# Kernel optimization log

Hardware: AMD Instinct MI355X
Metric: run time of the kernel (lower is better)

Reference implementation:

```python
import jax, jax.numpy as jnp
import numpy as np

G = 128          # resolution
NE = 4           # n_emotions
SIGMA = 0.05     # splat kernel width
ETA = 0.01       # global write strength
ALPHA_H = 0.002
ALPHA_E = 0.001
LEAK = 5e-05
RADIUS = max(2, int(3.0 * SIGMA * G / 2.0))   # = 9
W = 2 * RADIUS + 1                            # = 19


def _laplacian(x):
    # 6-neighbor Laplacian with replicate padding; x: [..., G, G, G]
    pad = [(0, 0)] * (x.ndim - 3) + [(1, 1)] * 3
    p = jnp.pad(x, pad, mode='edge')
    c = p[..., 1:-1, 1:-1, 1:-1]
    return (p[..., :-2, 1:-1, 1:-1] + p[..., 2:, 1:-1, 1:-1]
            + p[..., 1:-1, :-2, 1:-1] + p[..., 1:-1, 2:, 1:-1]
            + p[..., 1:-1, 1:-1, :-2] + p[..., 1:-1, 1:-1, 2:]
            - 6.0 * c)


def _splat(H, E, positions, intensities, emotions):
    # Gaussian splat scatter-add into H [G,G,G] and E [NE,G,G,G].
    gp = (positions + 1.0) * 0.5 * (G - 1)                       # [N,3] grid coords
    c = jnp.clip(jnp.floor(gp).astype(jnp.int32), 0, G - 1)      # center cell
    offs = jnp.arange(-RADIUS, RADIUS + 1, dtype=jnp.int32)
    coords = c[:, :, None] + offs[None, None, :]                 # [N,3,W]
    valid = (coords >= 0) & (coords < G)
    cc = jnp.clip(coords, 0, G - 1)
    sig = SIGMA * G / 2.0
    d = coords.astype(gp.dtype) - gp[:, :, None]                 # [N,3,W]
    k1 = jnp.where(valid, jnp.exp(-(d * d) / (2.0 * sig * sig)), 0.0)
    kx, ky, kz = k1[:, 0], k1[:, 1], k1[:, 2]                    # [N,W] each (separable)
    omega = intensities * ETA                                    # [N]
    vals = (omega[:, None, None, None] * kx[:, :, None, None]
            * ky[:, None, :, None] * kz[:, None, None, :])       # [N,W,W,W]
    flat = ((cc[:, 0][:, :, None, None] * G + cc[:, 1][:, None, :, None]) * G
            + cc[:, 2][:, None, None, :]).reshape(-1)            # [N*W^3]
    H_new = H.reshape(-1).at[flat].add(vals.reshape(-1)).reshape(G, G, G)
    E_ch = []
    for e in range(NE):
        ve = (vals * emotions[:, e][:, None, None, None]).reshape(-1)
        E_ch.append(E[e].reshape(-1).at[flat].add(ve).reshape(G, G, G))
    return H_new, jnp.stack(E_ch)


def _step(H, E):
    H2 = jnp.maximum(H * (1.0 - LEAK) + ALPHA_H * _laplacian(H), 0.0)
    E2 = jnp.maximum(E * (1.0 - LEAK) + LEAK + ALPHA_E * _laplacian(E), 0.0)
    return H2, E2


def _sample(H, E, sp):
    # grid_sample trilinear, padding_mode='border', align_corners=True.
    # grid_sample axis convention: sp[...,0]->last axis, sp[...,1]->middle, sp[...,2]->first.
    B, T, _ = sp.shape
    t = jnp.clip((sp.reshape(-1, 3) + 1.0) * 0.5 * (G - 1), 0.0, G - 1)  # [BT,3]
    i0 = jnp.floor(t).astype(jnp.int32)
    f = t - i0
    i0 = jnp.clip(i0, 0, G - 1)
    i1 = jnp.clip(i0 + 1, 0, G - 1)
    x0, y0, z0 = i0[:, 0], i0[:, 1], i0[:, 2]
    x1, y1, z1 = i1[:, 0], i1[:, 1], i1[:, 2]
    fx, fy, fz = f[:, 0], f[:, 1], f[:, 2]

    def interp(vol):  # vol [..., G,G,G] -> [..., BT]
        out = 0.0
        for zi, wz in ((z0, 1.0 - fz), (z1, fz)):
            for yi, wy in ((y0, 1.0 - fy), (y1, fy)):
                for xi, wx in ((x0, 1.0 - fx), (x1, fx)):
                    out = out + vol[..., zi, yi, xi] * (wz * wy * wx)
        return out

    p_H = interp(H).reshape(B, T)
    p_E = interp(E).T.reshape(B, T, NE)
    return p_H, p_E


def setup_inputs() -> dict:
    key = jax.random.key(0)
    k1, k2, k3, k4 = jax.random.split(key, 4)
    N, B, T = 4096, 8, 1024
    return {
        'positions': jax.random.uniform(k1, (N, 3), jnp.float32, -0.95, 0.95),
        'intensities': jax.random.uniform(k2, (N,), jnp.float32),
        'emotions': jax.random.uniform(k3, (N, NE), jnp.float32),
        'sample_positions': jax.random.uniform(k4, (B, T, 3), jnp.float32, -1.0, 1.0),
        'H0': jnp.zeros((G, G, G), jnp.float32),
        'E0': jnp.ones((NE, G, G, G), jnp.float32),
    }


def reference(positions, intensities, emotions, sample_positions, H0, E0):
    H, E = _splat(H0, E0, positions, intensities, emotions)
    H, E = _step(H, E)
    p_H, p_E = _sample(H, E, sample_positions)
    return jnp.concatenate([p_H[..., None], p_E], axis=-1)  # [B,T,1+NE]
```

## Files before the change

### kernel.cpp

```cpp
#include <hip/hip_runtime.h>


namespace {
constexpr int   G      = 128;
constexpr int   G3     = G * G * G;
constexpr int   RAD    = 9;
constexpr float SIG    = 0.05f * (float)G * 0.5f;
constexpr float INV2S2 = 1.0f / (2.0f * SIG * SIG);
constexpr float ETA    = 0.01f;
constexpr float A_H    = 0.002f;
constexpr float A_E    = 0.001f;
constexpr float LEAK   = 5e-5f;

constexpr int T0 = 8, T1 = 4, T2 = 16;
constexpr int NT0 = G / T0, NT1 = G / T1, NT2 = G / T2;
constexpr int NTILES = NT0 * NT1 * NT2;
constexpr int CAP  = 96;
constexpr int CSTR = 32;
}

__device__ __forceinline__ int clampi(int v, int lo, int hi) {
    return min(max(v, lo), hi);
}

__global__ void __launch_bounds__(256) bin_meta_kernel(
        const float* __restrict__ pos, const float* __restrict__ inten,
        const float4* __restrict__ emo4,
        int* __restrict__ counts, int* __restrict__ lists,
        float4* __restrict__ meta, int N) {
    const int p    = blockIdx.x * 4 + (threadIdx.x >> 6);
    const int lane = threadIdx.x & 63;
    if (p >= N) return;

    const float gx = (pos[p * 3 + 0] + 1.0f) * 0.5f * (float)(G - 1);
    const float gy = (pos[p * 3 + 1] + 1.0f) * 0.5f * (float)(G - 1);
    const float gz = (pos[p * 3 + 2] + 1.0f) * 0.5f * (float)(G - 1);
    const int c0 = clampi((int)floorf(gx), 0, G - 1);
    const int c1 = clampi((int)floorf(gy), 0, G - 1);
    const int c2 = clampi((int)floorf(gz), 0, G - 1);

    if (lane == 0) {
        meta[2 * p]     = make_float4(gx, gy, gz, inten[p] * ETA);
        meta[2 * p + 1] = emo4[p];
    }

    const int t0lo = (max(c0 - 18, 0) + T0 - 1) >> 3;
    const int t0hi = min(c0 + 10, G - 1) >> 3;
    const int t1lo = (max(c1 - 14, 0) + T1 - 1) >> 2;
    const int t1hi = min(c1 + 10, G - 1) >> 2;
    const int t2lo = (max(c2 - 26, 0) + T2 - 1) >> 4;
    const int t2hi = min(c2 + 10, G - 1) >> 4;
    const int n0 = t0hi - t0lo, n1 = t1hi - t1lo, n2 = t2hi - t2lo;

    for (int s = lane; s < 84; s += 64) {
        const int a  = s / 21;
        const int r  = s - a * 21;
        const int b  = r / 3;
        const int cs = r - b * 3;
        if (a <= n0 && b <= n1 && cs <= n2) {
            const int t = ((t0lo + a) * NT1 + (t1lo + b)) * NT2 + (t2lo + cs);
            const int slot = atomicAdd(&counts[t * CSTR], 1);
            if (slot < CAP) lists[t * CAP + slot] = p;
        }
    }
}

__device__ __forceinline__ float stepped_at(const float* __restrict__ vol,
                                            int z, int y, int x,
                                            float addc, float alpha) {
    const int zm = max(z - 1, 0), zp = min(z + 1, G - 1);
    const int ym = max(y - 1, 0), yp = min(y + 1, G - 1);
    const int xm = max(x - 1, 0), xp = min(x + 1, G - 1);
    const float cv  = vol[(z * G + y) * G + x];
    const float lap = vol[(zm * G + y) * G + x] + vol[(zp * G + y) * G + x]
                    + vol[(z * G + ym) * G + x] + vol[(z * G + yp) * G + x]
                    + vol[(z * G + y) * G + xm] + vol[(z * G + y) * G + xp]
                    - 6.0f * cv;
    return cv * (1.0f - LEAK) + addc + alpha * lap;
}

__device__ __forceinline__ void axis_eval(float g, int ia, int ib,
        int ma, int pa, int mb, int pb, float wa, float wb,
        float& dir, float& lap) {
    const int cp = clampi((int)floorf(g), 0, G - 1);
    auto kf = [&](int v) -> float {
        const float d = (float)v - g;
        const float e = __expf(-d * d * INV2S2);
        return (abs(v - cp) <= RAD) ? e : 0.0f;
    };
    const float ka = kf(ia), kb = kf(ib);
    lap = wa * (kf(ma) + kf(pa) - 2.0f * ka)
        + wb * (kf(mb) + kf(pb) - 2.0f * kb);
    dir = wa * ka + wb * kb;
}

__global__ void __launch_bounds__(256) fused_sample_kernel(
        const float* __restrict__ sp, const float4* __restrict__ meta,
        const int* __restrict__ counts, const int* __restrict__ lists,
        const float* __restrict__ H0, const float* __restrict__ E0,
        float* __restrict__ out, int n_samp) {
    const int wave = (blockIdx.x * blockDim.x + threadIdx.x) >> 6;
    const int lane = threadIdx.x & 63;
    if (wave >= n_samp) return;

    const float s0 = sp[wave * 3 + 0];
    const float s1 = sp[wave * 3 + 1];
    const float s2 = sp[wave * 3 + 2];
    const float uz = fminf(fmaxf((s2 + 1.0f) * 0.5f * (float)(G - 1), 0.0f), (float)(G - 1));
    const float uy = fminf(fmaxf((s1 + 1.0f) * 0.5f * (float)(G - 1), 0.0f), (float)(G - 1));
    const float ux = fminf(fmaxf((s0 + 1.0f) * 0.5f * (float)(G - 1), 0.0f), (float)(G - 1));
    const int za = (int)floorf(uz); const float fz = uz - (float)za;
    const int ya = (int)floorf(uy); const float fy = uy - (float)ya;
    const int xa = (int)floorf(ux); const float fx = ux - (float)xa;
    const int zb = min(za + 1, G - 1);
    const int yb = min(ya + 1, G - 1);
    const int xb = min(xa + 1, G - 1);

    float bv = 0.0f;
    if (lane < 40) {
        const int c = lane >> 3, corner = lane & 7;
        const int d0 = corner & 1, d1 = (corner >> 1) & 1, d2 = corner >> 2;
        const int x = d0 ? xb : xa, y = d1 ? yb : ya, z = d2 ? zb : za;
        const float w = (d0 ? fx : 1.0f - fx) * (d1 ? fy : 1.0f - fy)
                      * (d2 ? fz : 1.0f - fz);
        const float* vol  = (c == 0) ? H0 : E0 + (size_t)(c - 1) * G3;
        const float addc  = (c == 0) ? 0.0f : LEAK;
        const float alpha = (c == 0) ? A_H : A_E;
        bv = w * stepped_at(vol, z, y, x, addc, alpha);
    }
    bv += __shfl_xor(bv, 1);
    bv += __shfl_xor(bv, 2);
    bv += __shfl_xor(bv, 4);

    const int tile = ((za >> 3) * NT1 + (ya >> 2)) * NT2 + (xa >> 4);
    const int cnt = min(counts[tile * CSTR], CAP);
    const int* __restrict__ lst = lists + tile * CAP;

    const int zma = max(za - 1, 0), zpa = min(za + 1, G - 1);
    const int zmb = max(zb - 1, 0), zpb = min(zb + 1, G - 1);
    const int yma = max(ya - 1, 0), ypa = min(ya + 1, G - 1);
    const int ymb = max(yb - 1, 0), ypb = min(yb + 1, G - 1);
    const int xma = max(xa - 1, 0), xpa = min(xa + 1, G - 1);
    const int xmb = max(xb - 1, 0), xpb = min(xb + 1, G - 1);
    const float wza = 1.0f - fz, wzb = fz;
    const float wya = 1.0f - fy, wyb = fy;
    const float wxa = 1.0f - fx, wxb = fx;

    float aH = 0.0f, aE0 = 0.0f, aE1 = 0.0f, aE2 = 0.0f, aE3 = 0.0f;
    for (int nb = lane; nb < cnt; nb += 64) {
        const int p = lst[nb];
        const float4 mg = meta[2 * p];
        const float4 me = meta[2 * p + 1];
        float dz_, lz_, dy_, ly_, dx_, lx_;
        axis_eval(mg.x, za, zb, zma, zpa, zmb, zpb, wza, wzb, dz_, lz_);
        axis_eval(mg.y, ya, yb, yma, ypa, ymb, ypb, wya, wyb, dy_, ly_);
        axis_eval(mg.z, xa, xb, xma, xpa, xmb, xpb, wxa, wxb, dx_, lx_);
        const float b3 = dz_ * dy_ * dx_;
        const float l3 = lz_ * dy_ * dx_ + dz_ * ly_ * dx_ + dz_ * dy_ * lx_;
        const float cH = mg.w * ((1.0f - LEAK) * b3 + A_H * l3);
        const float cE = mg.w * ((1.0f - LEAK) * b3 + A_E * l3);
        aH  += cH;
        aE0 += cE * me.x;  aE1 += cE * me.y;
        aE2 += cE * me.z;  aE3 += cE * me.w;
    }

#define RED64(v) { v += __shfl_xor(v, 1);  v += __shfl_xor(v, 2);  \
                   v += __shfl_xor(v, 4);  v += __shfl_xor(v, 8);  \
                   v += __shfl_xor(v, 16); v += __shfl_xor(v, 32); }
    RED64(aH) RED64(aE0) RED64(aE1) RED64(aE2) RED64(aE3)
#undef RED64

    const int  src   = (lane < 5) ? lane * 8 : 0;
    const float basec = __shfl(bv, src);
    const float sv = (lane == 0) ? aH  : (lane == 1) ? aE0
                   : (lane == 2) ? aE1 : (lane == 3) ? aE2 : aE3;
    if (lane < 5) out[wave * 5 + lane] = basec + sv;
}

extern "C" void kernel_launch(void* const* d_in, const int* in_sizes, int n_in,
                              void* d_out, int out_size, void* d_ws, size_t ws_size,
                              hipStream_t stream) {
    const float* positions   = (const float*)d_in[0];
    const float* intensities = (const float*)d_in[1];
    const float* emotions    = (const float*)d_in[2];
    const float* sample_pos  = (const float*)d_in[3];
    const float* H0          = (const float*)d_in[4];
    const float* E0          = (const float*)d_in[5];
    float* out = (float*)d_out;

    const int N = in_sizes[0] / 3;

    int*    counts = (int*)d_ws;
    int*    lists  = counts + (size_t)NTILES * CSTR;
    float4* meta   = (float4*)(lists + (size_t)NTILES * CAP);

    hipMemsetAsync(counts, 0, (size_t)NTILES * CSTR * sizeof(int), stream);

    bin_meta_kernel<<<(N + 3) / 4, 256, 0, stream>>>(
        positions, intensities, (const float4*)emotions, counts, lists, meta, N);

    const int n_samp = out_size / 5;
    fused_sample_kernel<<<(n_samp + 3) / 4, 256, 0, stream>>>(
        sample_pos, meta, counts, lists, H0, E0, out, n_samp);
}
```

Measured before the change: 113.8 us.

## Move base-field sampling into binning kernel and trim splat-axis exp evaluations

Merges the binning work and the sampling of the stepped base volumes (H0/E0 Laplacian with interpolation) into one launch, using separate block ranges. This lets the memory-bound base gathers overlap with the atomic binning, and the second kernel then only adds splat contributions into the output with a read-modify-write. The per-axis kernel evaluation now reuses shared neighbour values, cutting six exponentials per axis down to four. The cost is an extra global read-modify-write of the output and the base-sample coordinate math done twice.

```diff
diff --git a/kernel.cpp b/kernel.cpp
--- a/kernel.cpp
+++ b/kernel.cpp
@@ -21,48 +21,6 @@
 
 __device__ __forceinline__ int clampi(int v, int lo, int hi) {
     return min(max(v, lo), hi);
-}
-
-__global__ void __launch_bounds__(256) bin_meta_kernel(
-        const float* __restrict__ pos, const float* __restrict__ inten,
-        const float4* __restrict__ emo4,
-        int* __restrict__ counts, int* __restrict__ lists,
-        float4* __restrict__ meta, int N) {
-    const int p    = blockIdx.x * 4 + (threadIdx.x >> 6);
-    const int lane = threadIdx.x & 63;
-    if (p >= N) return;
-
-    const float gx = (pos[p * 3 + 0] + 1.0f) * 0.5f * (float)(G - 1);
-    const float gy = (pos[p * 3 + 1] + 1.0f) * 0.5f * (float)(G - 1);
-    const float gz = (pos[p * 3 + 2] + 1.0f) * 0.5f * (float)(G - 1);
-    const int c0 = clampi((int)floorf(gx), 0, G - 1);
-    const int c1 = clampi((int)floorf(gy), 0, G - 1);
-    const int c2 = clampi((int)floorf(gz), 0, G - 1);
-
-    if (lane == 0) {
-        meta[2 * p]     = make_float4(gx, gy, gz, inten[p] * ETA);
-        meta[2 * p + 1] = emo4[p];
-    }
-
-    const int t0lo = (max(c0 - 18, 0) + T0 - 1) >> 3;
-    const int t0hi = min(c0 + 10, G - 1) >> 3;
-    const int t1lo = (max(c1 - 14, 0) + T1 - 1) >> 2;
-    const int t1hi = min(c1 + 10, G - 1) >> 2;
-    const int t2lo = (max(c2 - 26, 0) + T2 - 1) >> 4;
-    const int t2hi = min(c2 + 10, G - 1) >> 4;
-    const int n0 = t0hi - t0lo, n1 = t1hi - t1lo, n2 = t2hi - t2lo;
-
-    for (int s = lane; s < 84; s += 64) {
-        const int a  = s / 21;
-        const int r  = s - a * 21;
-        const int b  = r / 3;
-        const int cs = r - b * 3;
-        if (a <= n0 && b <= n1 && cs <= n2) {
-            const int t = ((t0lo + a) * NT1 + (t1lo + b)) * NT2 + (t2lo + cs);
-            const int slot = atomicAdd(&counts[t * CSTR], 1);
-            if (slot < CAP) lists[t * CAP + slot] = p;
-        }
-    }
 }
 
 __device__ __forceinline__ float stepped_at(const float* __restrict__ vol,
@@ -79,33 +37,61 @@
     return cv * (1.0f - LEAK) + addc + alpha * lap;
 }
 
-__device__ __forceinline__ void axis_eval(float g, int ia, int ib,
-        int ma, int pa, int mb, int pb, float wa, float wb,
-        float& dir, float& lap) {
-    const int cp = clampi((int)floorf(g), 0, G - 1);
-    auto kf = [&](int v) -> float {
-        const float d = (float)v - g;
-        const float e = __expf(-d * d * INV2S2);
-        return (abs(v - cp) <= RAD) ? e : 0.0f;
-    };
-    const float ka = kf(ia), kb = kf(ib);
-    lap = wa * (kf(ma) + kf(pa) - 2.0f * ka)
-        + wb * (kf(mb) + kf(pb) - 2.0f * kb);
-    dir = wa * ka + wb * kb;
-}
-
-__global__ void __launch_bounds__(256) fused_sample_kernel(
-        const float* __restrict__ sp, const float4* __restrict__ meta,
-        const int* __restrict__ counts, const int* __restrict__ lists,
+__global__ void __launch_bounds__(256) bin_base_kernel(
+        const float* __restrict__ pos, const float* __restrict__ inten,
+        const float4* __restrict__ emo4,
+        int* __restrict__ counts, int* __restrict__ lists,
+        float4* __restrict__ meta,
+        const float* __restrict__ sp,
         const float* __restrict__ H0, const float* __restrict__ E0,
-        float* __restrict__ out, int n_samp) {
-    const int wave = (blockIdx.x * blockDim.x + threadIdx.x) >> 6;
+        float* __restrict__ out,
+        int N, int nbin, int n_samp) {
     const int lane = threadIdx.x & 63;
-    if (wave >= n_samp) return;
-
-    const float s0 = sp[wave * 3 + 0];
-    const float s1 = sp[wave * 3 + 1];
-    const float s2 = sp[wave * 3 + 2];
+
+    if ((int)blockIdx.x < nbin) {
+        const int p = blockIdx.x * 4 + (threadIdx.x >> 6);
+        if (p >= N) return;
+
+        const float gx = (pos[p * 3 + 0] + 1.0f) * 0.5f * (float)(G - 1);
+        const float gy = (pos[p * 3 + 1] + 1.0f) * 0.5f * (float)(G - 1);
+        const float gz = (pos[p * 3 + 2] + 1.0f) * 0.5f * (float)(G - 1);
+        const int c0 = clampi((int)floorf(gx), 0, G - 1);
+        const int c1 = clampi((int)floorf(gy), 0, G - 1);
+        const int c2 = clampi((int)floorf(gz), 0, G - 1);
+
+        if (lane == 0) {
+            meta[2 * p]     = make_float4(gx, gy, gz, inten[p] * ETA);
+            meta[2 * p + 1] = emo4[p];
+        }
+
+        const int t0lo = (max(c0 - 18, 0) + T0 - 1) >> 3;
+        const int t0hi = min(c0 + 10, G - 1) >> 3;
+        const int t1lo = (max(c1 - 14, 0) + T1 - 1) >> 2;
+        const int t1hi = min(c1 + 10, G - 1) >> 2;
+        const int t2lo = (max(c2 - 26, 0) + T2 - 1) >> 4;
+        const int t2hi = min(c2 + 10, G - 1) >> 4;
+        const int n0 = t0hi - t0lo, n1 = t1hi - t1lo, n2 = t2hi - t2lo;
+
+        for (int s = lane; s < 84; s += 64) {
+            const int a  = s / 21;
+            const int r  = s - a * 21;
+            const int b  = r / 3;
+            const int cs = r - b * 3;
+            if (a <= n0 && b <= n1 && cs <= n2) {
+                const int t = ((t0lo + a) * NT1 + (t1lo + b)) * NT2 + (t2lo + cs);
+                const int slot = atomicAdd(&counts[t * CSTR], 1);
+                if (slot < CAP) lists[t * CAP + slot] = p;
+            }
+        }
+        return;
+    }
+
+    const int w = (blockIdx.x - nbin) * 4 + (threadIdx.x >> 6);
+    if (w >= n_samp) return;
+
+    const float s0 = sp[w * 3 + 0];
+    const float s1 = sp[w * 3 + 1];
+    const float s2 = sp[w * 3 + 2];
     const float uz = fminf(fmaxf((s2 + 1.0f) * 0.5f * (float)(G - 1), 0.0f), (float)(G - 1));
     const float uy = fminf(fmaxf((s1 + 1.0f) * 0.5f * (float)(G - 1), 0.0f), (float)(G - 1));
     const float ux = fminf(fmaxf((s0 + 1.0f) * 0.5f * (float)(G - 1), 0.0f), (float)(G - 1));
@@ -121,27 +107,60 @@
         const int c = lane >> 3, corner = lane & 7;
         const int d0 = corner & 1, d1 = (corner >> 1) & 1, d2 = corner >> 2;
         const int x = d0 ? xb : xa, y = d1 ? yb : ya, z = d2 ? zb : za;
-        const float w = (d0 ? fx : 1.0f - fx) * (d1 ? fy : 1.0f - fy)
-                      * (d2 ? fz : 1.0f - fz);
+        const float wt = (d0 ? fx : 1.0f - fx) * (d1 ? fy : 1.0f - fy)
+                       * (d2 ? fz : 1.0f - fz);
         const float* vol  = (c == 0) ? H0 : E0 + (size_t)(c - 1) * G3;
         const float addc  = (c == 0) ? 0.0f : LEAK;
         const float alpha = (c == 0) ? A_H : A_E;
-        bv = w * stepped_at(vol, z, y, x, addc, alpha);
+        bv = wt * stepped_at(vol, z, y, x, addc, alpha);
     }
     bv += __shfl_xor(bv, 1);
     bv += __shfl_xor(bv, 2);
     bv += __shfl_xor(bv, 4);
+    if (lane < 40 && (lane & 7) == 0) out[w * 5 + (lane >> 3)] = bv;
+}
+
+__device__ __forceinline__ void axis_eval4(float g, int ia, int ib,
+        float wa, float wb, float& dir, float& lap) {
+    const int cp = clampi((int)floorf(g), 0, G - 1);
+    const int ma = max(ia - 1, 0);
+    const int pb = min(ib + 1, G - 1);
+    auto kf = [&](int v) -> float {
+        const float d = (float)v - g;
+        const float e = __expf(-d * d * INV2S2);
+        return (abs(v - cp) <= RAD) ? e : 0.0f;
+    };
+    const float kma = kf(ma), ka = kf(ia), kb = kf(ib), kpb = kf(pb);
+    const float kmb = (ib > ia) ? ka : kma;
+    dir = wa * ka + wb * kb;
+    lap = wa * (kma + kb - 2.0f * ka) + wb * (kmb + kpb - 2.0f * kb);
+}
+
+__global__ void __launch_bounds__(256) splat_add_kernel(
+        const float* __restrict__ sp, const float4* __restrict__ meta,
+        const int* __restrict__ counts, const int* __restrict__ lists,
+        float* __restrict__ out, int n_samp) {
+    const int w = (blockIdx.x * blockDim.x + threadIdx.x) >> 6;
+    const int lane = threadIdx.x & 63;
+    if (w >= n_samp) return;
+
+    const float s0 = sp[w * 3 + 0];
+    const float s1 = sp[w * 3 + 1];
+    const float s2 = sp[w * 3 + 2];
+    const float uz = fminf(fmaxf((s2 + 1.0f) * 0.5f * (float)(G - 1), 0.0f), (float)(G - 1));
+    const float uy = fminf(fmaxf((s1 + 1.0f) * 0.5f * (float)(G - 1), 0.0f), (float)(G - 1));
+    const float ux = fminf(fmaxf((s0 + 1.0f) * 0.5f * (float)(G - 1), 0.0f), (float)(G - 1));
+    const int za = (int)floorf(uz); const float fz = uz - (float)za;
+    const int ya = (int)floorf(uy); const float fy = uy - (float)ya;
+    const int xa = (int)floorf(ux); const float fx = ux - (float)xa;
+    const int zb = min(za + 1, G - 1);
+    const int yb = min(ya + 1, G - 1);
+    const int xb = min(xa + 1, G - 1);
 
     const int tile = ((za >> 3) * NT1 + (ya >> 2)) * NT2 + (xa >> 4);
     const int cnt = min(counts[tile * CSTR], CAP);
     const int* __restrict__ lst = lists + tile * CAP;
 
-    const int zma = max(za - 1, 0), zpa = min(za + 1, G - 1);
-    const int zmb = max(zb - 1, 0), zpb = min(zb + 1, G - 1);
-    const int yma = max(ya - 1, 0), ypa = min(ya + 1, G - 1);
-    const int ymb = max(yb - 1, 0), ypb = min(yb + 1, G - 1);
-    const int xma = max(xa - 1, 0), xpa = min(xa + 1, G - 1);
-    const int xmb = max(xb - 1, 0), xpb = min(xb + 1, G - 1);
     const float wza = 1.0f - fz, wzb = fz;
     const float wya = 1.0f - fy, wyb = fy;
     const float wxa = 1.0f - fx, wxb = fx;
@@ -152,13 +171,14 @@
         const float4 mg = meta[2 * p];
         const float4 me = meta[2 * p + 1];
         float dz_, lz_, dy_, ly_, dx_, lx_;
-        axis_eval(mg.x, za, zb, zma, zpa, zmb, zpb, wza, wzb, dz_, lz_);
-        axis_eval(mg.y, ya, yb, yma, ypa, ymb, ypb, wya, wyb, dy_, ly_);
-        axis_eval(mg.z, xa, xb, xma, xpa, xmb, xpb, wxa, wxb, dx_, lx_);
+        axis_eval4(mg.x, za, zb, wza, wzb, dz_, lz_);
+        axis_eval4(mg.y, ya, yb, wya, wyb, dy_, ly_);
+        axis_eval4(mg.z, xa, xb, wxa, wxb, dx_, lx_);
         const float b3 = dz_ * dy_ * dx_;
         const float l3 = lz_ * dy_ * dx_ + dz_ * ly_ * dx_ + dz_ * dy_ * lx_;
-        const float cH = mg.w * ((1.0f - LEAK) * b3 + A_H * l3);
-        const float cE = mg.w * ((1.0f - LEAK) * b3 + A_E * l3);
+        const float bl = (1.0f - LEAK) * b3;
+        const float cH = mg.w * (bl + A_H * l3);
+        const float cE = mg.w * (bl + A_E * l3);
         aH  += cH;
         aE0 += cE * me.x;  aE1 += cE * me.y;
         aE2 += cE * me.z;  aE3 += cE * me.w;
@@ -170,11 +190,11 @@
     RED64(aH) RED64(aE0) RED64(aE1) RED64(aE2) RED64(aE3)
 #undef RED64
 
-    const int  src   = (lane < 5) ? lane * 8 : 0;
-    const float basec = __shfl(bv, src);
-    const float sv = (lane == 0) ? aH  : (lane == 1) ? aE0
-                   : (lane == 2) ? aE1 : (lane == 3) ? aE2 : aE3;
-    if (lane < 5) out[wave * 5 + lane] = basec + sv;
+    if (lane < 5) {
+        const float sv = (lane == 0) ? aH  : (lane == 1) ? aE0
+                       : (lane == 2) ? aE1 : (lane == 3) ? aE2 : aE3;
+        out[w * 5 + lane] += sv;
+    }
 }
 
 extern "C" void kernel_launch(void* const* d_in, const int* in_sizes, int n_in,
@@ -189,6 +209,7 @@
     float* out = (float*)d_out;
 
     const int N = in_sizes[0] / 3;
+    const int n_samp = out_size / 5;
 
     int*    counts = (int*)d_ws;
     int*    lists  = counts + (size_t)NTILES * CSTR;
@@ -196,10 +217,12 @@
 
     hipMemsetAsync(counts, 0, (size_t)NTILES * CSTR * sizeof(int), stream);
 
-    bin_meta_kernel<<<(N + 3) / 4, 256, 0, stream>>>(
-        positions, intensities, (const float4*)emotions, counts, lists, meta, N);
-
-    const int n_samp = out_size / 5;
-    fused_sample_kernel<<<(n_samp + 3) / 4, 256, 0, stream>>>(
-        sample_pos, meta, counts, lists, H0, E0, out, n_samp);
-}
+    const int nbin  = (N + 3) / 4;
+    const int nbase = (n_samp + 3) / 4;
+    bin_base_kernel<<<nbin + nbase, 256, 0, stream>>>(
+        positions, intensities, (const float4*)emotions,
+        counts, lists, meta, sample_pos, H0, E0, out, N, nbin, n_samp);
+
+    splat_add_kernel<<<(n_samp + 3) / 4, 256, 0, stream>>>(
+        sample_pos, meta, counts, lists, out, n_samp);
+}
```

Measured after the change: 112.3 us. Within noise of the previous version (-1.3%).
